# Optimization experiments

Measured on AMD Instinct MI355X. Metric: run time of the kernel, lower is better.

The kernel has to match this reference:

```python
import jax, jax.numpy as jnp
import numpy as np

L, B, S, H, O, IN = 8, 512, 128, 1024, 1024, 1024


def setup_inputs() -> dict:
    key = jax.random.key(0)
    ks = jax.random.split(key, 16)
    x = jax.random.normal(ks[0], (B, S, IN), dtype=jnp.float32)
    h_prev = jnp.zeros((L, B, H), dtype=jnp.float32)
    def w(k, shape):
        return jax.random.normal(k, shape, dtype=jnp.float32) * 0.01
    # input_size == hidden_size, so all layers stack into [L, ., .]
    W_xz = w(ks[1], (L, H, H)); W_hz = w(ks[2], (L, H, H)); b_z = jnp.zeros((L, H), jnp.float32)
    W_xr = w(ks[3], (L, H, H)); W_hr = w(ks[4], (L, H, H)); b_r = jnp.zeros((L, H), jnp.float32)
    W_xh = w(ks[5], (L, H, H)); W_hh = w(ks[6], (L, H, H)); b_h = jnp.zeros((L, H), jnp.float32)
    W_hy = w(ks[7], (H, O)); b_y = jnp.zeros((O,), jnp.float32)
    return {"x": x, "h_prev": h_prev, "W_xz": W_xz, "W_hz": W_hz, "b_z": b_z,
            "W_xr": W_xr, "W_hr": W_hr, "b_r": b_r, "W_xh": W_xh, "W_hh": W_hh,
            "b_h": b_h, "W_hy": W_hy, "b_y": b_y}


def reference(x, h_prev, W_xz, W_hz, b_z, W_xr, W_hr, b_r, W_xh, W_hh, b_h, W_hy, b_y):
    # Faithful to source: timestep loop runs over num_layers (= L) steps (source bug kept).
    nlayers = W_xz.shape[0]
    h = [h_prev[l] for l in range(nlayers)]  # per-layer hidden state [B, H]
    outputs, h_seq = [], []
    for t in range(nlayers):
        inp = x[:, t, :]
        for l in range(nlayers):
            hp = h[l]
            z = jax.nn.sigmoid(inp @ W_xz[l] + hp @ W_hz[l] + b_z[l])
            r = jax.nn.sigmoid(inp @ W_xr[l] + hp @ W_hr[l] + b_r[l])
            # note: (r * hp) @ W_hh matches python operator precedence in source
            h_tilde = jnp.tanh(inp @ W_xh[l] + (r * hp) @ W_hh[l] + b_h[l])
            h[l] = (1.0 - z) * hp + z * h_tilde
            inp = h[l]  # next layer sees this timestep's updated state
        outputs.append(h[-1] @ W_hy + b_y)
        h_seq.append(jnp.stack(h, axis=0))
    outputs = jnp.stack(outputs, axis=1)          # [B, T, O]
    h_seq_stacked = jnp.stack(h_seq, axis=1)      # [L, T, B, H]
    h_current = jnp.stack(h, axis=0)              # [L, B, H]
    return outputs, h_seq_stacked, h_current
```

## Files before the change

kernel.cpp:

```cpp
#include <hip/hip_runtime.h>
#include <hip/hip_bf16.h>

typedef __bf16 bf16;
typedef __attribute__((ext_vector_type(8))) __bf16 bf16x8;
typedef __attribute__((ext_vector_type(4))) __bf16 bf16x4;
typedef __attribute__((ext_vector_type(4))) float f32x4;

constexpr int kH = 1024;
constexpr int kB = 512;
constexpr int kT = 8;
constexpr int kL = 8;
constexpr int kS = 128;
constexpr size_t SL = (size_t)kB * kH;

constexpr int BM = 64, BN = 128, BK = 64;

__device__ __forceinline__ float sigmoidf_(float v) { return 1.0f / (1.0f + __expf(-v)); }

__device__ __forceinline__ int xcd_swizzle(int g, int nwg) {
  int q = nwg >> 3, r = nwg & 7;
  int xcd = g & 7, idx = g >> 3;
  return (xcd < r ? xcd * (q + 1) : r * (q + 1) + (xcd - r) * q) + idx;
}

template <int ROWS>
__device__ __forceinline__ void stage_tile(const bf16* __restrict__ src, int stride,
                                           bf16* lds, int tid) {
#pragma unroll
  for (int i = 0; i < ROWS / 32; ++i) {
    int seg = i * 256 + tid;
    int row = seg >> 3;
    int c8 = (seg & 7) * 8;
    __builtin_amdgcn_global_load_lds(
        (const __attribute__((address_space(1))) void*)(src + (size_t)row * stride + c8),
        (__attribute__((address_space(3))) void*)(lds + seg * 8),
        16, 0, 0);
  }
}

__device__ __forceinline__ void mma_step(const bf16* sA, const bf16* sB,
                                         f32x4 acc[2][4], int lane, int wr, int wc) {
  int frow = lane & 15, fko = (lane >> 4) * 8;
#pragma unroll
  for (int kk = 0; kk < 2; ++kk) {
    bf16x8 a[2], b[4];
#pragma unroll
    for (int m = 0; m < 2; ++m)
      a[m] = *(const bf16x8*)&sA[(wr * 32 + m * 16 + frow) * BK + kk * 32 + fko];
#pragma unroll
    for (int n = 0; n < 4; ++n)
      b[n] = *(const bf16x8*)&sB[(wc * 64 + n * 16 + frow) * BK + kk * 32 + fko];
#pragma unroll
    for (int m = 0; m < 2; ++m)
#pragma unroll
      for (int n = 0; n < 4; ++n)
        acc[m][n] = __builtin_amdgcn_mfma_f32_16x16x32_bf16(a[m], b[n], acc[m][n], 0, 0, 0);
  }
}

__global__ __launch_bounds__(256) void cvt_inputs(
    const float* __restrict__ x, const float* __restrict__ hprev,
    bf16* __restrict__ xb, bf16* __restrict__ hpb) {
  size_t i = ((size_t)blockIdx.x * 256 + threadIdx.x) * 4;
  if (blockIdx.y == 0) {
    size_t t = i >> 19, r = i & (SL - 1), b = r >> 10, h = r & 1023;
    float4 v = *(const float4*)(x + ((b * kS + t) << 10) + h);
    bf16x4 o = {(bf16)v.x, (bf16)v.y, (bf16)v.z, (bf16)v.w};
    *(bf16x4*)(xb + i) = o;
  } else {
    float4 v = *(const float4*)(hprev + i);
    bf16x4 o = {(bf16)v.x, (bf16)v.y, (bf16)v.z, (bf16)v.w};
    *(bf16x4*)(hpb + i) = o;
  }
}

__global__ __launch_bounds__(256) void wconv(
    const float* __restrict__ Wxz, const float* __restrict__ Whz,
    const float* __restrict__ Wxr, const float* __restrict__ Whr,
    const float* __restrict__ Wxh, const float* __restrict__ Whh,
    const float* __restrict__ Why, bf16* __restrict__ wzr,
    bf16* __restrict__ wch, bf16* __restrict__ wy) {
  __shared__ float tile[64][65];
  int mat = blockIdx.z;
  const float* src;
  bf16* dst;
  size_t dstride;
  if (mat < 48) {
    int g = mat >> 3, l = mat & 7;
    const float* bases[6] = {Wxz, Whz, Wxr, Whr, Wxh, Whh};
    src = bases[g] + (size_t)l * kH * kH;
    int pair = g >> 1;
    int koff = (g & 1) * 1024;
    if (pair < 2) dst = wzr + ((size_t)(pair * 8 + l)) * kH * 2048 + koff;
    else          dst = wch + (size_t)l * kH * 2048 + koff;
    dstride = 2048;
  } else {
    src = Why; dst = wy; dstride = 1024;
  }
  int k0 = blockIdx.x * 64;
  int n0 = blockIdx.y * 64;
  int tid = threadIdx.x;
  int cl = (tid & 15) * 4;
  int rw = tid >> 4;
#pragma unroll
  for (int i = 0; i < 4; ++i) {
    int r = rw + i * 16;
    float4 v = *(const float4*)(src + (size_t)(k0 + r) * kH + n0 + cl);
    tile[r][cl] = v.x; tile[r][cl + 1] = v.y; tile[r][cl + 2] = v.z; tile[r][cl + 3] = v.w;
  }
  __syncthreads();
#pragma unroll
  for (int p = 0; p < 2; ++p) {
    int idx = p * 256 + tid;
    int n = idx >> 3;
    int ko = (idx & 7) * 8;
    bf16x8 o;
#pragma unroll
    for (int i = 0; i < 8; ++i) o[i] = (bf16)tile[ko + i][n];
    *(bf16x8*)(dst + (size_t)(n0 + n) * dstride + k0 + ko) = o;
  }
}

__global__ __launch_bounds__(256, 4) void gru_zr(
    const bf16* __restrict__ xb, const bf16* __restrict__ hpb,
    const bf16* __restrict__ hb, const bf16* __restrict__ wzr,
    const float* __restrict__ b_z, const float* __restrict__ b_r,
    bf16* __restrict__ Zs, bf16* __restrict__ RHs, int diag, int t_lo) {
  __shared__ alignas(16) bf16 sA[BM * BK];
  __shared__ alignas(16) bf16 sB[BN * BK];
  int w = xcd_swizzle(blockIdx.x, gridDim.x);
  int bm0 = (w & 7) * BM;
  int bn0 = ((w >> 3) & 7) * BN;
  int gate = (w >> 6) & 1;
  int cell = w >> 7;
  int t = t_lo + cell, l = diag - t;
  int pprev = (diag - 1) & 1;
  const bf16* inpb = (l == 0) ? xb + (size_t)t * SL
                              : hb + (size_t)(pprev * 8 + (l - 1)) * SL;
  const bf16* hpbp = (t == 0) ? hpb + (size_t)l * SL
                              : hb + (size_t)(pprev * 8 + l) * SL;
  const bf16* wB = wzr + (size_t)(gate * 8 + l) * kH * 2048;

  int tid = threadIdx.x, lane = tid & 63, wv = tid >> 6;
  int wr = wv >> 1, wc = wv & 1;
  f32x4 acc[2][4] = {};

  for (int k0 = 0; k0 < 2048; k0 += BK) {
    const bf16* As = (k0 < 1024) ? inpb + (size_t)bm0 * kH + k0
                                 : hpbp + (size_t)bm0 * kH + (k0 - 1024);
    stage_tile<BM>(As, kH, sA, tid);
    stage_tile<BN>(wB + (size_t)bn0 * 2048 + k0, 2048, sB, tid);
    __syncthreads();
    mma_step(sA, sB, acc, lane, wr, wc);
    __syncthreads();
  }

  const float* bias = gate ? b_r : b_z;
  int frow = lane & 15, rb = (lane >> 4) * 4;
  bf16* Zc = Zs + (size_t)cell * SL;
  bf16* RHc = RHs + (size_t)cell * SL;
#pragma unroll
  for (int n = 0; n < 4; ++n) {
    int gcol = bn0 + wc * 64 + n * 16 + frow;
    float bv = bias[l * kH + gcol];
#pragma unroll
    for (int m = 0; m < 2; ++m) {
#pragma unroll
      for (int q = 0; q < 4; ++q) {
        int grow = bm0 + wr * 32 + m * 16 + rb + q;
        size_t off = (size_t)grow * kH + gcol;
        float v = sigmoidf_(acc[m][n][q] + bv);
        if (gate == 0) Zc[off] = (bf16)v;
        else           RHc[off] = (bf16)(v * (float)hpbp[off]);
      }
    }
  }
}

__global__ __launch_bounds__(256, 4) void gru_ch(
    const bf16* __restrict__ xb, bf16* __restrict__ hb,
    const float* __restrict__ hprevf, float* __restrict__ hseq,
    float* __restrict__ hcur, bf16* __restrict__ hb7,
    const bf16* __restrict__ wch, const float* __restrict__ b_h,
    const bf16* __restrict__ Zs, const bf16* __restrict__ RHs,
    int diag, int t_lo) {
  __shared__ alignas(16) bf16 sA[BM * BK];
  __shared__ alignas(16) bf16 sB[BN * BK];
  int w = xcd_swizzle(blockIdx.x, gridDim.x);
  int bm0 = (w & 7) * BM;
  int bn0 = ((w >> 3) & 7) * BN;
  int cell = w >> 6;
  int t = t_lo + cell, l = diag - t;
  int pprev = (diag - 1) & 1, pcur = diag & 1;
  const bf16* inpb = (l == 0) ? xb + (size_t)t * SL
                              : hb + (size_t)(pprev * 8 + (l - 1)) * SL;
  const bf16* RHc = RHs + (size_t)cell * SL;
  const bf16* Zc = Zs + (size_t)cell * SL;
  const float* hpf = (t == 0) ? hprevf + (size_t)l * SL
                              : hseq + (size_t)(l * kT + t - 1) * SL;
  float* hout = hseq + (size_t)(l * kT + t) * SL;
  bf16* hbout = hb + (size_t)(pcur * 8 + l) * SL;
  const bf16* wB = wch + (size_t)l * kH * 2048;

  int tid = threadIdx.x, lane = tid & 63, wv = tid >> 6;
  int wr = wv >> 1, wc = wv & 1;
  f32x4 acc[2][4] = {};

  for (int k0 = 0; k0 < 2048; k0 += BK) {
    const bf16* As = (k0 < 1024) ? inpb + (size_t)bm0 * kH + k0
                                 : RHc + (size_t)bm0 * kH + (k0 - 1024);
    stage_tile<BM>(As, kH, sA, tid);
    stage_tile<BN>(wB + (size_t)bn0 * 2048 + k0, 2048, sB, tid);
    __syncthreads();
    mma_step(sA, sB, acc, lane, wr, wc);
    __syncthreads();
  }

  int frow = lane & 15, rb = (lane >> 4) * 4;
  bool lastT = (t == kT - 1);
  bool lastL = (l == kL - 1);
#pragma unroll
  for (int n = 0; n < 4; ++n) {
    int gcol = bn0 + wc * 64 + n * 16 + frow;
    float bh = b_h[l * kH + gcol];
#pragma unroll
    for (int m = 0; m < 2; ++m) {
#pragma unroll
      for (int q = 0; q < 4; ++q) {
        int grow = bm0 + wr * 32 + m * 16 + rb + q;
        size_t off = (size_t)grow * kH + gcol;
        float ht = tanhf(acc[m][n][q] + bh);
        float z = (float)Zc[off];
        float hpv = hpf[off];
        float hn = (1.0f - z) * hpv + z * ht;
        hout[off] = hn;
        hbout[off] = (bf16)hn;
        if (lastL) hb7[(size_t)t * SL + off] = (bf16)hn;
        if (lastT) hcur[(size_t)l * SL + off] = hn;
      }
    }
  }
}

__global__ __launch_bounds__(256, 4) void out_gemm(
    const bf16* __restrict__ hb7, const bf16* __restrict__ wy,
    const float* __restrict__ b_y, float* __restrict__ out) {
  __shared__ alignas(16) bf16 sA[BM * BK];
  __shared__ alignas(16) bf16 sB[BN * BK];
  int w = xcd_swizzle(blockIdx.x, gridDim.x);
  int bm0 = (w & 63) * BM;
  int bn0 = (w >> 6) * BN;
  int tid = threadIdx.x, lane = tid & 63, wv = tid >> 6;
  int wr = wv >> 1, wc = wv & 1;
  f32x4 acc[2][4] = {};
  for (int k0 = 0; k0 < kH; k0 += BK) {
    stage_tile<BM>(hb7 + (size_t)bm0 * kH + k0, kH, sA, tid);
    stage_tile<BN>(wy + (size_t)bn0 * kH + k0, kH, sB, tid);
    __syncthreads();
    mma_step(sA, sB, acc, lane, wr, wc);
    __syncthreads();
  }
  int frow = lane & 15, rb = (lane >> 4) * 4;
#pragma unroll
  for (int n = 0; n < 4; ++n) {
    int gcol = bn0 + wc * 64 + n * 16 + frow;
    float by = b_y[gcol];
#pragma unroll
    for (int m = 0; m < 2; ++m) {
#pragma unroll
      for (int q = 0; q < 4; ++q) {
        int grow = bm0 + wr * 32 + m * 16 + rb + q;
        int tt = grow >> 9, bb = grow & 511;
        out[((size_t)bb * kT + tt) * kH + gcol] = acc[m][n][q] + by;
      }
    }
  }
}

extern "C" void kernel_launch(void* const* d_in, const int* in_sizes, int n_in,
                              void* d_out, int out_size, void* d_ws, size_t ws_size,
                              hipStream_t stream) {
  const float* x     = (const float*)d_in[0];
  const float* hprev = (const float*)d_in[1];
  const float* Wxz   = (const float*)d_in[2];
  const float* Whz   = (const float*)d_in[3];
  const float* bz    = (const float*)d_in[4];
  const float* Wxr   = (const float*)d_in[5];
  const float* Whr   = (const float*)d_in[6];
  const float* br    = (const float*)d_in[7];
  const float* Wxh   = (const float*)d_in[8];
  const float* Whh   = (const float*)d_in[9];
  const float* bh    = (const float*)d_in[10];
  const float* Why   = (const float*)d_in[11];
  const float* by    = (const float*)d_in[12];

  float* out  = (float*)d_out;
  float* hseq = out + (size_t)kB * kT * kH;
  float* hcur = hseq + (size_t)kL * kT * kB * kH;

  char* p = (char*)d_ws;
  bf16* wzr = (bf16*)p;            p += (size_t)2 * 8 * kH * 2048 * 2;
  bf16* wch = (bf16*)p;            p += (size_t)8 * kH * 2048 * 2;
  bf16* wy  = (bf16*)p;            p += (size_t)kH * kH * 2;
  bf16* xb  = (bf16*)p;            p += (size_t)8 * SL * 2;
  bf16* hpb = (bf16*)p;            p += (size_t)8 * SL * 2;
  bf16* hb  = (bf16*)p;            p += (size_t)16 * SL * 2;
  bf16* hb7 = (bf16*)p;            p += (size_t)8 * SL * 2;
  bf16* Zs  = (bf16*)p;            p += (size_t)8 * SL * 2;
  bf16* RHs = (bf16*)p;

  cvt_inputs<<<dim3(4096, 2), 256, 0, stream>>>(x, hprev, xb, hpb);
  wconv<<<dim3(16, 16, 49), 256, 0, stream>>>(Wxz, Whz, Wxr, Whr, Wxh, Whh, Why,
                                              wzr, wch, wy);

  for (int dg = 0; dg <= 14; ++dg) {
    int t_lo = dg > 7 ? dg - 7 : 0;
    int t_hi = dg < 7 ? dg : 7;
    int nc = t_hi - t_lo + 1;
    gru_zr<<<dim3(nc * 128), 256, 0, stream>>>(xb, hpb, hb, wzr, bz, br,
                                               Zs, RHs, dg, t_lo);
    gru_ch<<<dim3(nc * 64), 256, 0, stream>>>(xb, hb, hprev, hseq, hcur, hb7,
                                              wch, bh, Zs, RHs, dg, t_lo);
  }

  out_gemm<<<dim3(512), 256, 0, stream>>>(hb7, wy, by, out);
}
```

Before: 1.540 ms.

## Fuse wavefront GRU launches into one persistent cooperative kernel with grid syncs

Replaces the 30 per-diagonal gru_zr/gru_ch launches and the final output GEMM with one cooperative persistent kernel. The kernel walks the diagonals internally, separating phases with grid.sync and thread fences, and assigns work units per XCD by hand instead of using the old swizzle. This is meant to remove per-launch overhead and tail gaps between the small dependent kernels. In exchange, the grid is capped by occupancy at 1024 blocks, launch bounds drop to 2 blocks, and grid-wide barriers add sync cost and may lower per-phase parallelism.

```diff
diff --git a/kernel.cpp b/kernel.cpp
--- a/kernel.cpp
+++ b/kernel.cpp
@@ -1,5 +1,8 @@
 #include <hip/hip_runtime.h>
 #include <hip/hip_bf16.h>
+#include <hip/hip_cooperative_groups.h>
+
+namespace cg = cooperative_groups;
 
 typedef __bf16 bf16;
 typedef __attribute__((ext_vector_type(8))) __bf16 bf16x8;
@@ -16,12 +19,6 @@
 constexpr int BM = 64, BN = 128, BK = 64;
 
 __device__ __forceinline__ float sigmoidf_(float v) { return 1.0f / (1.0f + __expf(-v)); }
-
-__device__ __forceinline__ int xcd_swizzle(int g, int nwg) {
-  int q = nwg >> 3, r = nwg & 7;
-  int xcd = g & 7, idx = g >> 3;
-  return (xcd < r ? xcd * (q + 1) : r * (q + 1) + (xcd - r) * q) + idx;
-}
 
 template <int ROWS>
 __device__ __forceinline__ void stage_tile(const bf16* __restrict__ src, int stride,
@@ -121,30 +118,31 @@
   }
 }
 
-__global__ __launch_bounds__(256, 4) void gru_zr(
-    const bf16* __restrict__ xb, const bf16* __restrict__ hpb,
-    const bf16* __restrict__ hb, const bf16* __restrict__ wzr,
-    const float* __restrict__ b_z, const float* __restrict__ b_r,
-    bf16* __restrict__ Zs, bf16* __restrict__ RHs, int diag, int t_lo) {
-  __shared__ alignas(16) bf16 sA[BM * BK];
-  __shared__ alignas(16) bf16 sB[BN * BK];
-  int w = xcd_swizzle(blockIdx.x, gridDim.x);
-  int bm0 = (w & 7) * BM;
-  int bn0 = ((w >> 3) & 7) * BN;
-  int gate = (w >> 6) & 1;
-  int cell = w >> 7;
+struct Prm {
+  const bf16* xb; const bf16* hpb; bf16* hb;
+  const float* hprevf; float* hseq; float* hcur; bf16* hb7;
+  const bf16* wzr; const bf16* wch; const bf16* wy;
+  const float* bz; const float* br; const float* bh; const float* by;
+  bf16* Zs; bf16* RHs; float* out;
+};
+
+__device__ __forceinline__ void zr_unit(const Prm& p, int u, int diag, int t_lo,
+                                        bf16* sA, bf16* sB, int tid) {
+  int lane = tid & 63, wv = tid >> 6;
+  int wr = wv >> 1, wc = wv & 1;
+  int bm0 = (u & 7) * BM;
+  int bn0 = ((u >> 3) & 7) * BN;
+  int gate = (u >> 6) & 1;
+  int cell = u >> 7;
   int t = t_lo + cell, l = diag - t;
   int pprev = (diag - 1) & 1;
-  const bf16* inpb = (l == 0) ? xb + (size_t)t * SL
-                              : hb + (size_t)(pprev * 8 + (l - 1)) * SL;
-  const bf16* hpbp = (t == 0) ? hpb + (size_t)l * SL
-                              : hb + (size_t)(pprev * 8 + l) * SL;
-  const bf16* wB = wzr + (size_t)(gate * 8 + l) * kH * 2048;
-
-  int tid = threadIdx.x, lane = tid & 63, wv = tid >> 6;
-  int wr = wv >> 1, wc = wv & 1;
+  const bf16* inpb = (l == 0) ? p.xb + (size_t)t * SL
+                              : p.hb + (size_t)(pprev * 8 + (l - 1)) * SL;
+  const bf16* hpbp = (t == 0) ? p.hpb + (size_t)l * SL
+                              : p.hb + (size_t)(pprev * 8 + l) * SL;
+  const bf16* wB = p.wzr + (size_t)(gate * 8 + l) * kH * 2048;
+
   f32x4 acc[2][4] = {};
-
   for (int k0 = 0; k0 < 2048; k0 += BK) {
     const bf16* As = (k0 < 1024) ? inpb + (size_t)bm0 * kH + k0
                                  : hpbp + (size_t)bm0 * kH + (k0 - 1024);
@@ -155,10 +153,10 @@
     __syncthreads();
   }
 
-  const float* bias = gate ? b_r : b_z;
+  const float* bias = gate ? p.br : p.bz;
   int frow = lane & 15, rb = (lane >> 4) * 4;
-  bf16* Zc = Zs + (size_t)cell * SL;
-  bf16* RHc = RHs + (size_t)cell * SL;
+  bf16* Zc = p.Zs + (size_t)cell * SL;
+  bf16* RHc = p.RHs + (size_t)cell * SL;
 #pragma unroll
   for (int n = 0; n < 4; ++n) {
     int gcol = bn0 + wc * 64 + n * 16 + frow;
@@ -177,35 +175,26 @@
   }
 }
 
-__global__ __launch_bounds__(256, 4) void gru_ch(
-    const bf16* __restrict__ xb, bf16* __restrict__ hb,
-    const float* __restrict__ hprevf, float* __restrict__ hseq,
-    float* __restrict__ hcur, bf16* __restrict__ hb7,
-    const bf16* __restrict__ wch, const float* __restrict__ b_h,
-    const bf16* __restrict__ Zs, const bf16* __restrict__ RHs,
-    int diag, int t_lo) {
-  __shared__ alignas(16) bf16 sA[BM * BK];
-  __shared__ alignas(16) bf16 sB[BN * BK];
-  int w = xcd_swizzle(blockIdx.x, gridDim.x);
-  int bm0 = (w & 7) * BM;
-  int bn0 = ((w >> 3) & 7) * BN;
-  int cell = w >> 6;
+__device__ __forceinline__ void ch_unit(const Prm& p, int u, int diag, int t_lo,
+                                        bf16* sA, bf16* sB, int tid) {
+  int lane = tid & 63, wv = tid >> 6;
+  int wr = wv >> 1, wc = wv & 1;
+  int bm0 = (u & 7) * BM;
+  int bn0 = ((u >> 3) & 7) * BN;
+  int cell = u >> 6;
   int t = t_lo + cell, l = diag - t;
   int pprev = (diag - 1) & 1, pcur = diag & 1;
-  const bf16* inpb = (l == 0) ? xb + (size_t)t * SL
-                              : hb + (size_t)(pprev * 8 + (l - 1)) * SL;
-  const bf16* RHc = RHs + (size_t)cell * SL;
-  const bf16* Zc = Zs + (size_t)cell * SL;
-  const float* hpf = (t == 0) ? hprevf + (size_t)l * SL
-                              : hseq + (size_t)(l * kT + t - 1) * SL;
-  float* hout = hseq + (size_t)(l * kT + t) * SL;
-  bf16* hbout = hb + (size_t)(pcur * 8 + l) * SL;
-  const bf16* wB = wch + (size_t)l * kH * 2048;
-
-  int tid = threadIdx.x, lane = tid & 63, wv = tid >> 6;
-  int wr = wv >> 1, wc = wv & 1;
+  const bf16* inpb = (l == 0) ? p.xb + (size_t)t * SL
+                              : p.hb + (size_t)(pprev * 8 + (l - 1)) * SL;
+  const bf16* RHc = p.RHs + (size_t)cell * SL;
+  const bf16* Zc = p.Zs + (size_t)cell * SL;
+  const float* hpf = (t == 0) ? p.hprevf + (size_t)l * SL
+                              : p.hseq + (size_t)(l * kT + t - 1) * SL;
+  float* hout = p.hseq + (size_t)(l * kT + t) * SL;
+  bf16* hbout = p.hb + (size_t)(pcur * 8 + l) * SL;
+  const bf16* wB = p.wch + (size_t)l * kH * 2048;
+
   f32x4 acc[2][4] = {};
-
   for (int k0 = 0; k0 < 2048; k0 += BK) {
     const bf16* As = (k0 < 1024) ? inpb + (size_t)bm0 * kH + k0
                                  : RHc + (size_t)bm0 * kH + (k0 - 1024);
@@ -222,7 +211,7 @@
 #pragma unroll
   for (int n = 0; n < 4; ++n) {
     int gcol = bn0 + wc * 64 + n * 16 + frow;
-    float bh = b_h[l * kH + gcol];
+    float bh = p.bh[l * kH + gcol];
 #pragma unroll
     for (int m = 0; m < 2; ++m) {
 #pragma unroll
@@ -235,27 +224,22 @@
         float hn = (1.0f - z) * hpv + z * ht;
         hout[off] = hn;
         hbout[off] = (bf16)hn;
-        if (lastL) hb7[(size_t)t * SL + off] = (bf16)hn;
-        if (lastT) hcur[(size_t)l * SL + off] = hn;
+        if (lastL) p.hb7[(size_t)t * SL + off] = (bf16)hn;
+        if (lastT) p.hcur[(size_t)l * SL + off] = hn;
       }
     }
   }
 }
 
-__global__ __launch_bounds__(256, 4) void out_gemm(
-    const bf16* __restrict__ hb7, const bf16* __restrict__ wy,
-    const float* __restrict__ b_y, float* __restrict__ out) {
-  __shared__ alignas(16) bf16 sA[BM * BK];
-  __shared__ alignas(16) bf16 sB[BN * BK];
-  int w = xcd_swizzle(blockIdx.x, gridDim.x);
-  int bm0 = (w & 63) * BM;
-  int bn0 = (w >> 6) * BN;
-  int tid = threadIdx.x, lane = tid & 63, wv = tid >> 6;
+__device__ __forceinline__ void out_unit(const Prm& p, int u, bf16* sA, bf16* sB, int tid) {
+  int lane = tid & 63, wv = tid >> 6;
   int wr = wv >> 1, wc = wv & 1;
+  int bm0 = (u & 63) * BM;
+  int bn0 = (u >> 6) * BN;
   f32x4 acc[2][4] = {};
   for (int k0 = 0; k0 < kH; k0 += BK) {
-    stage_tile<BM>(hb7 + (size_t)bm0 * kH + k0, kH, sA, tid);
-    stage_tile<BN>(wy + (size_t)bn0 * kH + k0, kH, sB, tid);
+    stage_tile<BM>(p.hb7 + (size_t)bm0 * kH + k0, kH, sA, tid);
+    stage_tile<BN>(p.wy + (size_t)bn0 * kH + k0, kH, sB, tid);
     __syncthreads();
     mma_step(sA, sB, acc, lane, wr, wc);
     __syncthreads();
@@ -264,17 +248,46 @@
 #pragma unroll
   for (int n = 0; n < 4; ++n) {
     int gcol = bn0 + wc * 64 + n * 16 + frow;
-    float by = b_y[gcol];
+    float by = p.by[gcol];
 #pragma unroll
     for (int m = 0; m < 2; ++m) {
 #pragma unroll
       for (int q = 0; q < 4; ++q) {
         int grow = bm0 + wr * 32 + m * 16 + rb + q;
         int tt = grow >> 9, bb = grow & 511;
-        out[((size_t)bb * kT + tt) * kH + gcol] = acc[m][n][q] + by;
+        p.out[((size_t)bb * kT + tt) * kH + gcol] = acc[m][n][q] + by;
       }
     }
   }
+}
+
+__global__ __launch_bounds__(256, 2) void gru_persist(Prm p) {
+  __shared__ alignas(16) bf16 sA[BM * BK];
+  __shared__ alignas(16) bf16 sB[BN * BK];
+  cg::grid_group grid = cg::this_grid();
+  int tid = threadIdx.x;
+  int bid = blockIdx.x;
+  int xcd = bid & 7, li = bid >> 3, nbx = gridDim.x >> 3;
+
+  for (int dg = 0; dg <= 14; ++dg) {
+    int t_lo = dg > 7 ? dg - 7 : 0;
+    int t_hi = dg < 7 ? dg : 7;
+    int nc = t_hi - t_lo + 1;
+    int cs = (nc * 128) >> 3;
+    for (int j = li; j < cs; j += nbx)
+      zr_unit(p, xcd * cs + j, dg, t_lo, sA, sB, tid);
+    __threadfence();
+    grid.sync();
+    __threadfence();
+    cs = (nc * 64) >> 3;
+    for (int j = li; j < cs; j += nbx)
+      ch_unit(p, xcd * cs + j, dg, t_lo, sA, sB, tid);
+    __threadfence();
+    grid.sync();
+    __threadfence();
+  }
+  for (int j = li; j < 64; j += nbx)
+    out_unit(p, xcd * 64 + j, sA, sB, tid);
 }
 
 extern "C" void kernel_launch(void* const* d_in, const int* in_sizes, int n_in,
@@ -313,15 +326,19 @@
   wconv<<<dim3(16, 16, 49), 256, 0, stream>>>(Wxz, Whz, Wxr, Whr, Wxh, Whh, Why,
                                               wzr, wch, wy);
 
-  for (int dg = 0; dg <= 14; ++dg) {
-    int t_lo = dg > 7 ? dg - 7 : 0;
-    int t_hi = dg < 7 ? dg : 7;
-    int nc = t_hi - t_lo + 1;
-    gru_zr<<<dim3(nc * 128), 256, 0, stream>>>(xb, hpb, hb, wzr, bz, br,
-                                               Zs, RHs, dg, t_lo);
-    gru_ch<<<dim3(nc * 64), 256, 0, stream>>>(xb, hb, hprev, hseq, hcur, hb7,
-                                              wch, bh, Zs, RHs, dg, t_lo);
-  }
-
-  out_gemm<<<dim3(512), 256, 0, stream>>>(hb7, wy, by, out);
-}
+  int nblk = 0;
+  hipOccupancyMaxActiveBlocksPerMultiprocessor(&nblk, gru_persist, 256, 0);
+  if (nblk < 1) nblk = 1;
+  int grid = nblk * 256;
+  if (grid > 1024) grid = 1024;
+
+  Prm prm;
+  prm.xb = xb; prm.hpb = hpb; prm.hb = hb;
+  prm.hprevf = hprev; prm.hseq = hseq; prm.hcur = hcur; prm.hb7 = hb7;
+  prm.wzr = wzr; prm.wch = wch; prm.wy = wy;
+  prm.bz = bz; prm.br = br; prm.bh = bh; prm.by = by;
+  prm.Zs = Zs; prm.RHs = RHs; prm.out = out;
+  void* kargs[] = {(void*)&prm};
+  hipLaunchCooperativeKernel((const void*)gru_persist, dim3(grid), dim3(256),
+                             kargs, 0, stream);
+}
```

Result: slower. 5.810 ms (+277.3%).
